# Optimization experiments

Hardware: AMD Instinct MI355X
Metric: run time of the kernel (lower is better)

## Reference

```python
import jax, jax.numpy as jnp
import numpy as np

B, T, C, H = 4, 1024, 1024, 16
HS = C // H  # head_size = 64
EPS = 1e-5


def layer_norm(x, w, b):
    mu = jnp.mean(x, axis=-1, keepdims=True)
    var = jnp.mean(jnp.square(x - mu), axis=-1, keepdims=True)
    return (x - mu) * jax.lax.rsqrt(var + EPS) * w + b


def setup_inputs() -> dict:
    key = jax.random.key(0)
    ks = jax.random.split(key, 12)
    s = 0.02
    return {
        "x": jax.random.normal(ks[0], (B, T, C), jnp.float32),
        "ln1_w": jnp.ones((C,), jnp.float32),
        "ln1_b": jnp.zeros((C,), jnp.float32),
        "Wk": jax.random.normal(ks[1], (H, C, HS), jnp.float32) * s,
        "Wq": jax.random.normal(ks[2], (H, C, HS), jnp.float32) * s,
        "Wv": jax.random.normal(ks[3], (H, C, HS), jnp.float32) * s,
        "Wo": jax.random.normal(ks[4], (C, C), jnp.float32) * s,
        "bo": jnp.zeros((C,), jnp.float32),
        "ln2_w": jnp.ones((C,), jnp.float32),
        "ln2_b": jnp.zeros((C,), jnp.float32),
        "W1": jax.random.normal(ks[5], (C, 4 * C), jnp.float32) * s,
        "b1": jnp.zeros((4 * C,), jnp.float32),
        "prelu_a": jnp.asarray(0.25, jnp.float32),
        "W2": jax.random.normal(ks[6], (4 * C, C), jnp.float32) * s,
        "b2": jnp.zeros((C,), jnp.float32),
    }


def reference(x, ln1_w, ln1_b, Wk, Wq, Wv, Wo, bo, ln2_w, ln2_b, W1, b1, prelu_a, W2, b2):
    # --- self-attention branch (pre-LN) ---
    h = layer_norm(x, ln1_w, ln1_b)  # [B,T,C]
    k = jnp.einsum('btc,hcd->bhtd', h, Wk)
    q = jnp.einsum('btc,hcd->bhtd', h, Wq)
    v = jnp.einsum('btc,hcd->bhtd', h, Wv)
    # NOTE: source computes k @ q^T (not q @ k^T) scaled by n_embd**-0.5
    wei = jnp.einsum('bhtd,bhsd->bhts', k, q) * (C ** -0.5)  # [B,H,T,T]
    causal = jnp.tril(jnp.ones((T, T), bool))
    wei = jnp.where(causal, wei, -jnp.inf)
    wei = jax.nn.softmax(wei, axis=-1)
    out = jnp.einsum('bhts,bhsd->bthd', wei, v).reshape(B, T, C)
    out = out @ Wo + bo
    x = x + out
    # --- feed-forward branch (pre-LN) ---
    h2 = layer_norm(x, ln2_w, ln2_b)
    f = h2 @ W1 + b1
    f = jnp.where(f > 0, f, prelu_a * f)  # PReLU, single scalar param
    f = f @ W2 + b2
    return x + f
```

## Files before the change

### kernel.cpp

```cpp
#include <hip/hip_runtime.h>


typedef __bf16 bf16_t;
typedef __attribute__((ext_vector_type(8))) __bf16 bfx8;
typedef __attribute__((ext_vector_type(4))) __bf16 bfx4;
typedef __attribute__((ext_vector_type(4))) float f32x4;
typedef __attribute__((ext_vector_type(8))) unsigned short u16x8;
typedef unsigned int u32;

#define MFMA_BF16(a, b, c) __builtin_amdgcn_mfma_f32_16x16x32_bf16((a), (b), (c), 0, 0, 0)
#define GLOAD_LDS16(g, l)                                                     \
  __builtin_amdgcn_global_load_lds((__attribute__((address_space(1))) void*)(g), \
                                   (__attribute__((address_space(3))) void*)(l), 16, 0, 0)

__global__ __launch_bounds__(256) void ln_kernel(const float* __restrict__ x,
                                                 const float* __restrict__ w,
                                                 const float* __restrict__ b,
                                                 bf16_t* __restrict__ out) {
  const int row = blockIdx.x;
  const int tid = threadIdx.x;
  const float4 v = reinterpret_cast<const float4*>(x + (size_t)row * 1024)[tid];
  float s = v.x + v.y + v.z + v.w;
  float s2 = v.x * v.x + v.y * v.y + v.z * v.z + v.w * v.w;
#pragma unroll
  for (int off = 1; off < 64; off <<= 1) {
    s += __shfl_xor(s, off);
    s2 += __shfl_xor(s2, off);
  }
  __shared__ float red[8];
  const int wv = tid >> 6;
  if ((tid & 63) == 0) {
    red[wv] = s;
    red[4 + wv] = s2;
  }
  __syncthreads();
  s = red[0] + red[1] + red[2] + red[3];
  s2 = red[4] + red[5] + red[6] + red[7];
  const float mu = s * (1.0f / 1024.0f);
  const float rs = rsqrtf(s2 * (1.0f / 1024.0f) - mu * mu + 1e-5f);
  const float4 wv4 = reinterpret_cast<const float4*>(w)[tid];
  const float4 bv4 = reinterpret_cast<const float4*>(b)[tid];
  bfx4 o;
  o[0] = (bf16_t)((v.x - mu) * rs * wv4.x + bv4.x);
  o[1] = (bf16_t)((v.y - mu) * rs * wv4.y + bv4.y);
  o[2] = (bf16_t)((v.z - mu) * rs * wv4.z + bv4.z);
  o[3] = (bf16_t)((v.w - mu) * rs * wv4.w + bv4.w);
  reinterpret_cast<bfx4*>(out + (size_t)row * 1024)[tid] = o;
}

__global__ __launch_bounds__(256) void transpose_cast(const float* __restrict__ in,
                                                      bf16_t* __restrict__ out, int K, int N,
                                                      long in_bstride, long out_bstride) {
  __shared__ float tile[64][65];
  const int z = blockIdx.z;
  in += (long)z * in_bstride;
  out += (long)z * out_bstride;
  const int k0 = blockIdx.x * 64, n0 = blockIdx.y * 64;
  const int t = threadIdx.x;
  const int rl = t >> 4, cl = (t & 15) * 4;
#pragma unroll
  for (int p = 0; p < 4; ++p) {
    const int r = p * 16 + rl;
    const float4 v = *reinterpret_cast<const float4*>(in + (size_t)(k0 + r) * N + n0 + cl);
    tile[r][cl] = v.x;
    tile[r][cl + 1] = v.y;
    tile[r][cl + 2] = v.z;
    tile[r][cl + 3] = v.w;
  }
  __syncthreads();
#pragma unroll
  for (int p = 0; p < 2; ++p) {
    const int idx = p * 256 + t;
    const int n = idx >> 3, kc = (idx & 7) * 8;
    bfx8 o;
#pragma unroll
    for (int i = 0; i < 8; ++i) o[i] = (bf16_t)tile[kc + i][n];
    *reinterpret_cast<bfx8*>(out + (size_t)(n0 + n) * K + k0 + kc) = o;
  }
}

enum { EPI_QKV = 0, EPI_WO = 1, EPI_MLP1 = 2, EPI_FINAL = 3 };

template <int EPI, int BM>
__global__ __launch_bounds__(256) void gemm_bt(
    const bf16_t* __restrict__ A, const bf16_t* __restrict__ BT,
    const float* __restrict__ bias, const float* __restrict__ res,
    const float* __restrict__ prelu, float* __restrict__ outf,
    bf16_t* __restrict__ ob0, bf16_t* __restrict__ ob1, bf16_t* __restrict__ ob2,
    int K, int N) {
  __shared__ __align__(16) bf16_t sA[BM * 64];
  __shared__ __align__(16) bf16_t sB[128 * 64];
  const int tid = threadIdx.x;
  const int lane = tid & 63;
  const int w = tid >> 6;
  const int wr = w >> 1, wc = w & 1;
  const int row0 = blockIdx.x * BM, col0 = blockIdx.y * 128;
  constexpr int MF = BM / 32;

  f32x4 acc[MF][4] = {};

  for (int k0 = 0; k0 < K; k0 += 64) {
    __syncthreads();
#pragma unroll
    for (int j = 0; j < MF; ++j) {
      const int chunk = j * 256 + tid;
      const int r = chunk >> 3, c = chunk & 7;
      const int cs = c ^ (r & 7);
      GLOAD_LDS16(A + (size_t)(row0 + r) * K + k0 + cs * 8, sA + chunk * 8);
    }
#pragma unroll
    for (int j = 0; j < 4; ++j) {
      const int chunk = j * 256 + tid;
      const int r = chunk >> 3, c = chunk & 7;
      const int cs = c ^ (r & 7);
      GLOAD_LDS16(BT + (size_t)(col0 + r) * K + k0 + cs * 8, sB + chunk * 8);
    }
    __syncthreads();
#pragma unroll
    for (int kk = 0; kk < 2; ++kk) {
      bfx8 af[MF], bfr[4];
#pragma unroll
      for (int m = 0; m < MF; ++m) {
        const int r = wr * (BM / 2) + m * 16 + (lane & 15);
        const int c = (kk * 4 + (lane >> 4)) ^ (r & 7);
        af[m] = *reinterpret_cast<const bfx8*>(sA + r * 64 + c * 8);
      }
#pragma unroll
      for (int n = 0; n < 4; ++n) {
        const int r = wc * 64 + n * 16 + (lane & 15);
        const int c = (kk * 4 + (lane >> 4)) ^ (r & 7);
        bfr[n] = *reinterpret_cast<const bfx8*>(sB + r * 64 + c * 8);
      }
#pragma unroll
      for (int m = 0; m < MF; ++m)
#pragma unroll
        for (int n = 0; n < 4; ++n) acc[m][n] = MFMA_BF16(af[m], bfr[n], acc[m][n]);
    }
  }

  const float pa = (EPI == EPI_MLP1) ? prelu[0] : 0.0f;
#pragma unroll
  for (int m = 0; m < MF; ++m) {
#pragma unroll
    for (int n = 0; n < 4; ++n) {
#pragma unroll
      for (int j = 0; j < 4; ++j) {
        const int row = row0 + wr * (BM / 2) + m * 16 + ((lane >> 4) << 2) + j;
        const int col = col0 + wc * 64 + n * 16 + (lane & 15);
        const float v = acc[m][n][j];
        if (EPI == EPI_QKV) {
          const int sel = col >> 10;
          const int h = (col >> 6) & 15, d = col & 63;
          const int bb = row >> 10, t = row & 1023;
          bf16_t* dst = (sel == 0) ? ob0 : (sel == 1) ? ob1 : ob2;
          dst[((size_t)(bb * 16 + h) * 1024 + t) * 64 + d] = (bf16_t)v;
        } else if (EPI == EPI_MLP1) {
          float t = v + bias[col];
          t = (t > 0.0f) ? t : pa * t;
          ob0[(size_t)row * N + col] = (bf16_t)t;
        } else {
          outf[(size_t)row * N + col] = v + bias[col] + res[(size_t)row * N + col];
        }
      }
    }
  }
}

__global__ __launch_bounds__(256) void attn_kernel(const bf16_t* __restrict__ kproj,
                                                   const bf16_t* __restrict__ qproj,
                                                   const bf16_t* __restrict__ vproj,
                                                   bf16_t* __restrict__ att) {
  __shared__ __align__(16) bf16_t sK[2][64 * 64];
  __shared__ __align__(16) bf16_t sVt[2][64 * 64];
  __shared__ __align__(16) bf16_t sP[4][16 * 64];
  const int tid = threadIdx.x, lane = tid & 63, w = tid >> 6;
  const int g = lane >> 4, l15 = lane & 15;
  const int bh = blockIdx.y;
  const size_t head = (size_t)bh * (1024 * 64);
  const int b = bh >> 4, h = bh & 15;
  const int vrow = 2 * (tid >> 3);
  const int vdb = tid & 7;

  for (int half = 0; half < 2; ++half) {
    const int tb = half ? (15 - (int)blockIdx.x) : (int)blockIdx.x;
    const int t0 = tb * 64;
    const int nsb = tb + 1;

    __syncthreads();

    bfx8 aq0, aq1;
    {
      const bf16_t* qrow = kproj + head + (size_t)(t0 + w * 16 + l15) * 64 + g * 8;
      aq0 = *reinterpret_cast<const bfx8*>(qrow);
      aq1 = *reinterpret_cast<const bfx8*>(qrow + 32);
    }

    {
#pragma unroll
      for (int j = 0; j < 2; ++j) {
        const int chunk = j * 256 + tid;
        const int r = chunk >> 3, c = chunk & 7;
        const int cs = c ^ (r & 7);
        GLOAD_LDS16(qproj + head + (size_t)r * 64 + cs * 8, sK[0] + chunk * 8);
      }
      const bf16_t* vp = vproj + head + (size_t)vrow * 64 + vdb * 8;
      const u16x8 v0 = *reinterpret_cast<const u16x8*>(vp);
      const u16x8 v1 = *reinterpret_cast<const u16x8*>(vp + 64);
#pragma unroll
      for (int i = 0; i < 8; ++i) {
        const int d = vdb * 8 + i;
        const int cc = ((vrow >> 3) ^ i ^ vdb) & 7;
        const u32 pk = ((u32)v1[i] << 16) | (u32)v0[i];
        *reinterpret_cast<u32*>(sVt[0] + d * 64 + cc * 8 + (vrow & 7)) = pk;
      }
    }
    __syncthreads();

    f32x4 accO[4] = {};
    float mrun[4], lrun[4];
#pragma unroll
    for (int j = 0; j < 4; ++j) {
      mrun[j] = -1e30f;
      lrun[j] = 0.0f;
    }

    for (int sb = 0; sb < nsb; ++sb) {
      const int cur = sb & 1;
      const bool pf = (sb + 1 < nsb);
      u16x8 v0n, v1n;
      if (pf) {
        const int s0n = (sb + 1) * 64;
#pragma unroll
        for (int j = 0; j < 2; ++j) {
          const int chunk = j * 256 + tid;
          const int r = chunk >> 3, c = chunk & 7;
          const int cs = c ^ (r & 7);
          GLOAD_LDS16(qproj + head + (size_t)(s0n + r) * 64 + cs * 8, sK[cur ^ 1] + chunk * 8);
        }
        const bf16_t* vp = vproj + head + (size_t)(s0n + vrow) * 64 + vdb * 8;
        v0n = *reinterpret_cast<const u16x8*>(vp);
        v1n = *reinterpret_cast<const u16x8*>(vp + 64);
      }

      f32x4 accS[4] = {};
      const bf16_t* sKc = sK[cur];
#pragma unroll
      for (int kk = 0; kk < 2; ++kk) {
        const bfx8 aq = kk ? aq1 : aq0;
#pragma unroll
        for (int n = 0; n < 4; ++n) {
          const int r = n * 16 + l15;
          const int c = (kk * 4 + g) ^ (r & 7);
          const bfx8 bk = *reinterpret_cast<const bfx8*>(sKc + r * 64 + c * 8);
          accS[n] = MFMA_BF16(aq, bk, accS[n]);
        }
      }

      const int rbase = t0 + w * 16 + (g << 2);
      const int cbase = sb * 64 + l15;
#pragma unroll
      for (int j = 0; j < 4; ++j) {
        const int t = rbase + j;
        float mx = -1e30f;
#pragma unroll
        for (int n = 0; n < 4; ++n) {
          float v = accS[n][j] * 0.03125f;
          v = ((cbase + n * 16) <= t) ? v : -1e30f;
          accS[n][j] = v;
          mx = fmaxf(mx, v);
        }
        mx = fmaxf(mx, __shfl_xor(mx, 1));
        mx = fmaxf(mx, __shfl_xor(mx, 2));
        mx = fmaxf(mx, __shfl_xor(mx, 4));
        mx = fmaxf(mx, __shfl_xor(mx, 8));
        const float mnew = fmaxf(mrun[j], mx);
        const float al = __expf(mrun[j] - mnew);
        float rsum = 0.0f;
#pragma unroll
        for (int n = 0; n < 4; ++n) {
          const float p = __expf(accS[n][j] - mnew);
          accS[n][j] = p;
          rsum += p;
        }
        rsum += __shfl_xor(rsum, 1);
        rsum += __shfl_xor(rsum, 2);
        rsum += __shfl_xor(rsum, 4);
        rsum += __shfl_xor(rsum, 8);
        lrun[j] = lrun[j] * al + rsum;
        mrun[j] = mnew;
#pragma unroll
        for (int n = 0; n < 4; ++n) accO[n][j] *= al;
      }

      bf16_t* sPw = sP[w];
#pragma unroll
      for (int n = 0; n < 4; ++n)
#pragma unroll
        for (int j = 0; j < 4; ++j) {
          const int r = (g << 2) + j;
          const int s = n * 16 + l15;
          const int cc = (s >> 3) ^ (r & 7);
          sPw[r * 64 + cc * 8 + (s & 7)] = (bf16_t)accS[n][j];
        }

      const bf16_t* sVc = sVt[cur];
#pragma unroll
      for (int kk = 0; kk < 2; ++kk) {
        bfx8 ap;
        {
          const int r = l15;
          const int c = (kk * 4 + g) ^ (r & 7);
          ap = *reinterpret_cast<const bfx8*>(sPw + r * 64 + c * 8);
        }
#pragma unroll
        for (int n = 0; n < 4; ++n) {
          const int d = n * 16 + l15;
          const int c = (kk * 4 + g) ^ (d & 7) ^ ((d >> 3) & 7);
          const bfx8 bv = *reinterpret_cast<const bfx8*>(sVc + d * 64 + c * 8);
          accO[n] = MFMA_BF16(ap, bv, accO[n]);
        }
      }

      if (pf) {
#pragma unroll
        for (int i = 0; i < 8; ++i) {
          const int d = vdb * 8 + i;
          const int cc = ((vrow >> 3) ^ i ^ vdb) & 7;
          const u32 pk = ((u32)v1n[i] << 16) | (u32)v0n[i];
          *reinterpret_cast<u32*>(sVt[cur ^ 1] + d * 64 + cc * 8 + (vrow & 7)) = pk;
        }
      }
      __syncthreads();
    }

#pragma unroll
    for (int j = 0; j < 4; ++j) {
      const float inv = 1.0f / lrun[j];
      const int t = t0 + w * 16 + (g << 2) + j;
#pragma unroll
      for (int n = 0; n < 4; ++n) {
        const int d = n * 16 + l15;
        att[((size_t)(b * 1024 + t)) * 1024 + h * 64 + d] = (bf16_t)(accO[n][j] * inv);
      }
    }
  }
}

extern "C" void kernel_launch(void* const* d_in, const int* in_sizes, int n_in,
                              void* d_out, int out_size, void* d_ws, size_t ws_size,
                              hipStream_t stream) {
  (void)in_sizes; (void)n_in; (void)out_size; (void)ws_size;
  const float* x = (const float*)d_in[0];
  const float* ln1w = (const float*)d_in[1];
  const float* ln1b = (const float*)d_in[2];
  const float* Wk = (const float*)d_in[3];
  const float* Wq = (const float*)d_in[4];
  const float* Wv = (const float*)d_in[5];
  const float* Wo = (const float*)d_in[6];
  const float* bo = (const float*)d_in[7];
  const float* ln2w = (const float*)d_in[8];
  const float* ln2b = (const float*)d_in[9];
  const float* W1 = (const float*)d_in[10];
  const float* b1 = (const float*)d_in[11];
  const float* pa = (const float*)d_in[12];
  const float* W2 = (const float*)d_in[13];
  const float* b2 = (const float*)d_in[14];
  float* out = (float*)d_out;
  char* ws = (char*)d_ws;
  const size_t MB = 1ull << 20;
  bf16_t* h1 = (bf16_t*)(ws + 0 * MB);
  bf16_t* h2 = (bf16_t*)(ws + 8 * MB);
  bf16_t* qb = (bf16_t*)(ws + 16 * MB);
  bf16_t* kb = (bf16_t*)(ws + 24 * MB);
  bf16_t* vb = (bf16_t*)(ws + 32 * MB);
  bf16_t* attb = (bf16_t*)(ws + 40 * MB);
  bf16_t* fbuf = (bf16_t*)(ws + 48 * MB);
  bf16_t* WqkvT = (bf16_t*)(ws + 80 * MB);
  bf16_t* WoT = (bf16_t*)(ws + 86 * MB);
  bf16_t* W1T = (bf16_t*)(ws + 88 * MB);
  bf16_t* W2T = (bf16_t*)(ws + 96 * MB);

  transpose_cast<<<dim3(16, 1, 16), 256, 0, stream>>>(Wq, WqkvT, 1024, 64, 65536, 65536);
  transpose_cast<<<dim3(16, 1, 16), 256, 0, stream>>>(Wk, WqkvT + (1024 * 1024), 1024, 64,
                                                      65536, 65536);
  transpose_cast<<<dim3(16, 1, 16), 256, 0, stream>>>(Wv, WqkvT + (2048 * 1024), 1024, 64,
                                                      65536, 65536);
  transpose_cast<<<dim3(16, 16, 1), 256, 0, stream>>>(Wo, WoT, 1024, 1024, 0, 0);
  transpose_cast<<<dim3(16, 64, 1), 256, 0, stream>>>(W1, W1T, 1024, 4096, 0, 0);
  transpose_cast<<<dim3(64, 16, 1), 256, 0, stream>>>(W2, W2T, 4096, 1024, 0, 0);

  ln_kernel<<<4096, 256, 0, stream>>>(x, ln1w, ln1b, h1);
  gemm_bt<EPI_QKV, 128><<<dim3(32, 24), 256, 0, stream>>>(h1, WqkvT, nullptr, nullptr,
                                                          nullptr, nullptr, qb, kb, vb,
                                                          1024, 3072);
  attn_kernel<<<dim3(8, 64), 256, 0, stream>>>(kb, qb, vb, attb);
  gemm_bt<EPI_WO, 64><<<dim3(64, 8), 256, 0, stream>>>(attb, WoT, bo, x, nullptr, out,
                                                       nullptr, nullptr, nullptr, 1024, 1024);
  ln_kernel<<<4096, 256, 0, stream>>>(out, ln2w, ln2b, h2);
  gemm_bt<EPI_MLP1, 128><<<dim3(32, 32), 256, 0, stream>>>(h2, W1T, b1, nullptr, pa, nullptr,
                                                           fbuf, nullptr, nullptr, 1024, 4096);
  gemm_bt<EPI_FINAL, 64><<<dim3(64, 8), 256, 0, stream>>>(fbuf, W2T, b2, out, nullptr, out,
                                                          nullptr, nullptr, nullptr, 4096, 1024);
}
```

Measured before the change: 238.3 us.

## Double-buffer GEMM LDS tiles and merge QKV weight transposes into one launch

The GEMM main loop now uses two LDS buffers, issuing the global-to-LDS loads for the next K tile before computing on the current one, so load latency overlaps MFMA work. It keeps one barrier per iteration instead of two. The three separate Q/K/V weight transpose launches are merged into a single kernel to cut launch overhead. Doubling LDS per block may lower occupancy, and there is no wait on the async LDS loads beyond the barrier.

```diff
diff --git a/kernel.cpp b/kernel.cpp
--- a/kernel.cpp
+++ b/kernel.cpp
@@ -48,15 +48,9 @@
   reinterpret_cast<bfx4*>(out + (size_t)row * 1024)[tid] = o;
 }
 
-__global__ __launch_bounds__(256) void transpose_cast(const float* __restrict__ in,
-                                                      bf16_t* __restrict__ out, int K, int N,
-                                                      long in_bstride, long out_bstride) {
-  __shared__ float tile[64][65];
-  const int z = blockIdx.z;
-  in += (long)z * in_bstride;
-  out += (long)z * out_bstride;
-  const int k0 = blockIdx.x * 64, n0 = blockIdx.y * 64;
-  const int t = threadIdx.x;
+__device__ __forceinline__ void tc_body(const float* __restrict__ in,
+                                        bf16_t* __restrict__ out, int K, int N, int k0,
+                                        int n0, float (*tile)[65], int t) {
   const int rl = t >> 4, cl = (t & 15) * 4;
 #pragma unroll
   for (int p = 0; p < 4; ++p) {
@@ -79,7 +73,47 @@
   }
 }
 
+__global__ __launch_bounds__(256) void transpose_cast(const float* __restrict__ in,
+                                                      bf16_t* __restrict__ out, int K,
+                                                      int N) {
+  __shared__ float tile[64][65];
+  tc_body(in, out, K, N, blockIdx.x * 64, blockIdx.y * 64, tile, threadIdx.x);
+}
+
+__global__ __launch_bounds__(256) void transpose_qkv(const float* __restrict__ Wq,
+                                                     const float* __restrict__ Wk,
+                                                     const float* __restrict__ Wv,
+                                                     bf16_t* __restrict__ out) {
+  __shared__ float tile[64][65];
+  const int z = blockIdx.y;
+  const int sel = z >> 4, h = z & 15;
+  const float* in = ((sel == 0) ? Wq : (sel == 1) ? Wk : Wv) + h * 65536;
+  bf16_t* o = out + (size_t)sel * 1048576 + h * 65536;
+  tc_body(in, o, 1024, 64, blockIdx.x * 64, 0, tile, threadIdx.x);
+}
+
 enum { EPI_QKV = 0, EPI_WO = 1, EPI_MLP1 = 2, EPI_FINAL = 3 };
+
+template <int MF>
+__device__ __forceinline__ void stage_tile(const bf16_t* __restrict__ A,
+                                           const bf16_t* __restrict__ BT, int K, int row0,
+                                           int col0, int k0, bf16_t* sA, bf16_t* sB,
+                                           int tid) {
+#pragma unroll
+  for (int j = 0; j < MF; ++j) {
+    const int chunk = j * 256 + tid;
+    const int r = chunk >> 3, c = chunk & 7;
+    const int cs = c ^ (r & 7);
+    GLOAD_LDS16(A + (size_t)(row0 + r) * K + k0 + cs * 8, sA + chunk * 8);
+  }
+#pragma unroll
+  for (int j = 0; j < 4; ++j) {
+    const int chunk = j * 256 + tid;
+    const int r = chunk >> 3, c = chunk & 7;
+    const int cs = c ^ (r & 7);
+    GLOAD_LDS16(BT + (size_t)(col0 + r) * K + k0 + cs * 8, sB + chunk * 8);
+  }
+}
 
 template <int EPI, int BM>
 __global__ __launch_bounds__(256) void gemm_bt(
@@ -88,34 +122,27 @@
     const float* __restrict__ prelu, float* __restrict__ outf,
     bf16_t* __restrict__ ob0, bf16_t* __restrict__ ob1, bf16_t* __restrict__ ob2,
     int K, int N) {
-  __shared__ __align__(16) bf16_t sA[BM * 64];
-  __shared__ __align__(16) bf16_t sB[128 * 64];
+  constexpr int MF = BM / 32;
+  __shared__ __align__(16) bf16_t sA[2][BM * 64];
+  __shared__ __align__(16) bf16_t sB[2][128 * 64];
   const int tid = threadIdx.x;
   const int lane = tid & 63;
   const int w = tid >> 6;
   const int wr = w >> 1, wc = w & 1;
   const int row0 = blockIdx.x * BM, col0 = blockIdx.y * 128;
-  constexpr int MF = BM / 32;
 
   f32x4 acc[MF][4] = {};
 
-  for (int k0 = 0; k0 < K; k0 += 64) {
-    __syncthreads();
-#pragma unroll
-    for (int j = 0; j < MF; ++j) {
-      const int chunk = j * 256 + tid;
-      const int r = chunk >> 3, c = chunk & 7;
-      const int cs = c ^ (r & 7);
-      GLOAD_LDS16(A + (size_t)(row0 + r) * K + k0 + cs * 8, sA + chunk * 8);
-    }
-#pragma unroll
-    for (int j = 0; j < 4; ++j) {
-      const int chunk = j * 256 + tid;
-      const int r = chunk >> 3, c = chunk & 7;
-      const int cs = c ^ (r & 7);
-      GLOAD_LDS16(BT + (size_t)(col0 + r) * K + k0 + cs * 8, sB + chunk * 8);
-    }
-    __syncthreads();
+  stage_tile<MF>(A, BT, K, row0, col0, 0, sA[0], sB[0], tid);
+  __syncthreads();
+
+  const int nk = K >> 6;
+  for (int t = 0; t < nk; ++t) {
+    const int cur = t & 1;
+    if (t + 1 < nk)
+      stage_tile<MF>(A, BT, K, row0, col0, (t + 1) * 64, sA[cur ^ 1], sB[cur ^ 1], tid);
+    const bf16_t* __restrict__ pA = sA[cur];
+    const bf16_t* __restrict__ pB = sB[cur];
 #pragma unroll
     for (int kk = 0; kk < 2; ++kk) {
       bfx8 af[MF], bfr[4];
@@ -123,19 +150,20 @@
       for (int m = 0; m < MF; ++m) {
         const int r = wr * (BM / 2) + m * 16 + (lane & 15);
         const int c = (kk * 4 + (lane >> 4)) ^ (r & 7);
-        af[m] = *reinterpret_cast<const bfx8*>(sA + r * 64 + c * 8);
+        af[m] = *reinterpret_cast<const bfx8*>(pA + r * 64 + c * 8);
       }
 #pragma unroll
       for (int n = 0; n < 4; ++n) {
         const int r = wc * 64 + n * 16 + (lane & 15);
         const int c = (kk * 4 + (lane >> 4)) ^ (r & 7);
-        bfr[n] = *reinterpret_cast<const bfx8*>(sB + r * 64 + c * 8);
+        bfr[n] = *reinterpret_cast<const bfx8*>(pB + r * 64 + c * 8);
       }
 #pragma unroll
       for (int m = 0; m < MF; ++m)
 #pragma unroll
         for (int n = 0; n < 4; ++n) acc[m][n] = MFMA_BF16(af[m], bfr[n], acc[m][n]);
     }
+    __syncthreads();
   }
 
   const float pa = (EPI == EPI_MLP1) ? prelu[0] : 0.0f;
@@ -380,14 +408,10 @@
   bf16_t* W1T = (bf16_t*)(ws + 88 * MB);
   bf16_t* W2T = (bf16_t*)(ws + 96 * MB);
 
-  transpose_cast<<<dim3(16, 1, 16), 256, 0, stream>>>(Wq, WqkvT, 1024, 64, 65536, 65536);
-  transpose_cast<<<dim3(16, 1, 16), 256, 0, stream>>>(Wk, WqkvT + (1024 * 1024), 1024, 64,
-                                                      65536, 65536);
-  transpose_cast<<<dim3(16, 1, 16), 256, 0, stream>>>(Wv, WqkvT + (2048 * 1024), 1024, 64,
-                                                      65536, 65536);
-  transpose_cast<<<dim3(16, 16, 1), 256, 0, stream>>>(Wo, WoT, 1024, 1024, 0, 0);
-  transpose_cast<<<dim3(16, 64, 1), 256, 0, stream>>>(W1, W1T, 1024, 4096, 0, 0);
-  transpose_cast<<<dim3(64, 16, 1), 256, 0, stream>>>(W2, W2T, 4096, 1024, 0, 0);
+  transpose_qkv<<<dim3(16, 48), 256, 0, stream>>>(Wq, Wk, Wv, WqkvT);
+  transpose_cast<<<dim3(16, 16), 256, 0, stream>>>(Wo, WoT, 1024, 1024);
+  transpose_cast<<<dim3(16, 64), 256, 0, stream>>>(W1, W1T, 1024, 4096);
+  transpose_cast<<<dim3(64, 16), 256, 0, stream>>>(W2, W2T, 4096, 1024);
 
   ln_kernel<<<4096, 256, 0, stream>>>(x, ln1w, ln1b, h1);
   gemm_bt<EPI_QKV, 128><<<dim3(32, 24), 256, 0, stream>>>(h1, WqkvT, nullptr, nullptr,
```

After: 227.1 us. 4.7% less time.
